# Optimization experiments

Hardware: AMD Instinct MI355X
Metric: run time of the kernel (lower is better)

The kernel has to match this reference:

```python
import jax, jax.numpy as jnp
import numpy as np

# Synthetic base image encoder: patchify(16) -> Linear(768,768)+ReLU -> Linear(768,3072)+ReLU -> mean-pool -> Linear(3072,512)
B, T = 32, 8          # batch, num task vectors
D, DH, F, MH = 768, 3072, 512, 128  # patch dim, hidden, feat_dim, meta-net hidden


def _patchify(x):
    # x: [B,3,224,224] -> [B,196,768] (14x14 patches of 16x16x3)
    Bn = x.shape[0]
    p = x.reshape(Bn, 3, 14, 16, 14, 16).transpose(0, 2, 4, 1, 3, 5)
    return p.reshape(Bn, 196, 768)


def _encode_shared(p, W1, b1, W2, b2, W3, b3):
    h = jax.nn.relu(p @ W1 + b1)          # [B,196,768]
    h2 = jax.nn.relu(h @ W2 + b2)         # [B,196,3072]
    return h2.mean(axis=1) @ W3 + b3      # [B,512]


def setup_inputs() -> dict:
    key = jax.random.key(0)
    ks = jax.random.split(key, 18)
    inp = {"x": jax.random.normal(ks[0], (B, 3, 224, 224), jnp.float32)}
    shapes = {
        "W1": (D, D), "b1": (D,), "W2": (D, DH), "b2": (DH,), "W3": (DH, F), "b3": (F,),
        "dW1": (T, D, D), "db1": (T, D), "dW2": (T, D, DH), "db2": (T, DH),
        "dW3": (T, DH, F), "db3": (T, F),
        "mW1": (F, MH), "mb1": (MH,), "mW2": (MH, T), "mb2": (T,),
    }
    for i, (n, sh) in enumerate(shapes.items()):
        inp[n] = jax.random.normal(ks[i + 1], sh, jnp.float32) * 0.02
    return inp


def reference(x, W1, b1, W2, b2, W3, b3, dW1, db1, dW2, db2, dW3, db3, mW1, mb1, mW2, mb2):
    p = _patchify(x)
    # base features computed with frozen params (torch.no_grad -> stop_gradient)
    base = jax.lax.stop_gradient(_encode_shared(p, W1, b1, W2, b2, W3, b3))
    # MetaNet: Linear-ReLU-Linear -> per-sample task-vector coefficients [B,T]
    coefs = jax.nn.relu(base @ mW1 + mb1) @ mW2 + mb2
    # per-sample composed parameters: theta_b = theta + sum_t coef[b,t] * dtheta_t
    W1b = W1 + jnp.einsum('bt,tde->bde', coefs, dW1)   # [B,768,768]
    b1b = b1 + coefs @ db1
    W2b = W2 + jnp.einsum('bt,tde->bde', coefs, dW2)   # [B,768,3072]
    b2b = b2 + coefs @ db2
    W3b = W3 + jnp.einsum('bt,tdf->bdf', coefs, dW3)   # [B,3072,512]
    b3b = b3 + coefs @ db3
    # batched per-sample forward (replaces the python loop over the batch)
    h = jax.nn.relu(jnp.einsum('bpd,bde->bpe', p, W1b) + b1b[:, None, :])
    h2 = jax.nn.relu(jnp.einsum('bpe,bef->bpf', h, W2b) + b2b[:, None, :])
    return jnp.einsum('be,bef->bf', h2.mean(axis=1), W3b) + b3b  # [B,512]
```

## Files before the change

kernel.cpp:

```cpp
#include <hip/hip_runtime.h>
#include <hip/hip_bf16.h>

#define BATCH 32
#define NPATCH 196
#define PD 768
#define DH 3072
#define FD 512
#define MH 128
#define NT 8

typedef unsigned short u16;
typedef u16   u16x8  __attribute__((ext_vector_type(8)));
typedef short bf16x8 __attribute__((ext_vector_type(8)));
typedef float f32x4  __attribute__((ext_vector_type(4)));

__device__ __forceinline__ void async16(const void* g, void* l)
{
    __builtin_amdgcn_global_load_lds(
        (const __attribute__((address_space(1))) void*)g,
        (__attribute__((address_space(3))) void*)l, 16, 0, 0);
}

#define BARRIER() do { asm volatile("" ::: "memory"); __builtin_amdgcn_s_barrier(); asm volatile("" ::: "memory"); } while (0)
#define VMWAIT(n) asm volatile("s_waitcnt vmcnt(" #n ")" ::: "memory")

#define GK  768
#define NK  24
#define GBM 256
#define GBN 128
#define GBK 32
#define ASZ (GBM*GBK)
#define BSZ (GBN*GBK)

__global__ __launch_bounds__(512, 4)
void gemm_bf16(const u16* __restrict__ A, const u16* __restrict__ BT,
               const float* __restrict__ bias, u16* __restrict__ C,
               float* __restrict__ pooled,
               int M, int N, long sA, long sB, long sC, long sBias,
               int relu, int pool)
{
    const int z = blockIdx.z;
    A  += (long)z * sA;
    BT += (long)z * sB;
    C  += (long)z * sC;
    const float* bz = bias ? bias + (long)z * sBias : nullptr;

    __shared__ __align__(16) u16 As[3 * ASZ];
    __shared__ __align__(16) u16 Bs[3 * BSZ];

    const int tid  = threadIdx.x;
    const int lane = tid & 63;
    const int wave = tid >> 6;
    const int wr = (wave >> 1) * 64;
    const int wc = (wave & 1) * 64;
    const int m0 = blockIdx.y * GBM;
    const int n0 = blockIdx.x * GBN;
    const int lrow = lane & 15;
    const int koff = (lane >> 4) * 8;

    f32x4 acc[4][4] = {};

    auto issue = [&](int kt, int bi) {
        u16* asb = As + bi * ASZ;
        u16* bsb = Bs + bi * BSZ;
        const int k0 = kt * GBK;
#pragma unroll
        for (int r = 0; r < 2; ++r) {
            int chunk = r * 512 + tid;
            int row = chunk >> 2;
            int k8  = chunk & 3;
            int gm  = m0 + row; if (gm >= M) gm = M - 1;
            async16(A + (long)gm * GK + k0 + k8 * 8,
                    asb + (size_t)(r * 512 + wave * 64) * 8);
        }
        int rowb = tid >> 2;
        int k8b  = tid & 3;
        async16(BT + (long)(n0 + rowb) * GK + k0 + k8b * 8,
                bsb + (size_t)(wave * 64) * 8);
    };

    auto compute = [&](int bi) {
        const u16* asb = As + bi * ASZ;
        const u16* bsb = Bs + bi * BSZ;
        bf16x8 af[4], bfr[4];
#pragma unroll
        for (int i = 0; i < 4; ++i)
            af[i] = *(const bf16x8*)(asb + (wr + i * 16 + lrow) * GBK + koff);
#pragma unroll
        for (int j = 0; j < 4; ++j)
            bfr[j] = *(const bf16x8*)(bsb + (wc + j * 16 + lrow) * GBK + koff);
#pragma unroll
        for (int i = 0; i < 4; ++i)
#pragma unroll
            for (int j = 0; j < 4; ++j)
                acc[i][j] = __builtin_amdgcn_mfma_f32_16x16x32_bf16(af[i], bfr[j], acc[i][j], 0, 0, 0);
    };

    issue(0, 0); issue(1, 1); issue(2, 2);

    for (int ii = 0; ii < 7; ++ii) {
        int i0 = ii * 3;
        VMWAIT(6); BARRIER(); compute(0); BARRIER(); issue(i0 + 3, 0);
        VMWAIT(6); BARRIER(); compute(1); BARRIER(); issue(i0 + 4, 1);
        VMWAIT(6); BARRIER(); compute(2); BARRIER(); issue(i0 + 5, 2);
    }
    VMWAIT(6); BARRIER(); compute(0); BARRIER();
    VMWAIT(3); BARRIER(); compute(1); BARRIER();
    VMWAIT(0); BARRIER(); compute(2);

    const int crow = (lane >> 4) * 4;
    const int ccol = lane & 15;

    if (!pool) {
#pragma unroll
        for (int j = 0; j < 4; ++j) {
            int gn = n0 + wc + j * 16 + ccol;
            float bv = bz ? bz[gn] : 0.f;
#pragma unroll
            for (int i = 0; i < 4; ++i) {
#pragma unroll
                for (int rg = 0; rg < 4; ++rg) {
                    int gm = m0 + wr + i * 16 + crow + rg;
                    if (gm < M) {
                        float v = acc[i][j][rg] + bv;
                        if (relu) v = fmaxf(v, 0.f);
                        __hip_bfloat16 hv = __float2bfloat16(v);
                        C[(long)gm * N + gn] = *(u16*)&hv;
                    }
                }
            }
        }
    } else {
        float* poolbuf = (float*)As;
        __syncthreads();
        const int slot = (wave >> 1) * 4 + (lane >> 4);
#pragma unroll
        for (int j = 0; j < 4; ++j) {
            int gn = n0 + wc + j * 16 + ccol;
            float bv = bz ? bz[gn] : 0.f;
            float s = 0.f;
#pragma unroll
            for (int i = 0; i < 4; ++i) {
#pragma unroll
                for (int rg = 0; rg < 4; ++rg) {
                    int gm = wr + i * 16 + crow + rg;
                    if (gm < NPATCH) s += fmaxf(acc[i][j][rg] + bv, 0.f);
                }
            }
            poolbuf[slot * 128 + wc + j * 16 + ccol] = s;
        }
        __syncthreads();
        if (tid < 128) {
            float s = 0.f;
#pragma unroll
            for (int q = 0; q < 16; ++q) s += poolbuf[q * 128 + tid];
            pooled[(long)z * N + n0 + tid] = s * (1.0f / NPATCH);
        }
    }
}

#define L3CHUNK 128

__global__ __launch_bounds__(256)
void skinny3(const float* __restrict__ A, const float* __restrict__ B0,
             const float* __restrict__ dB, const float* __restrict__ cf,
             float* __restrict__ outp, int kchunk)
{
    const int z  = blockIdx.y;
    const int k0 = blockIdx.z * kchunk;
    const float* B = (z == 0) ? B0 : dB + (long)(z - 1) * DH * FD;

    __shared__ float Asl[BATCH][L3CHUNK];

    const int tid = threadIdx.x;
    const int n   = blockIdx.x * 64 + (tid & 63);
    const int bg  = tid >> 6;

    float acc[8] = {};

    for (int kc = 0; kc < kchunk; kc += L3CHUNK) {
#pragma unroll
        for (int r = 0; r < 16; ++r) {
            int idx = tid + r * 256;
            int b = idx >> 7;
            int k = idx & 127;
            float s = (z == 0) ? 1.f : cf[b * NT + z - 1];
            Asl[b][k] = s * A[(long)b * DH + k0 + kc + k];
        }
        __syncthreads();
#pragma unroll 4
        for (int k = 0; k < L3CHUNK; ++k) {
            float w = B[(long)(k0 + kc + k) * FD + n];
#pragma unroll
            for (int bb = 0; bb < 8; ++bb)
                acc[bb] = fmaf(Asl[bg * 8 + bb][k], w, acc[bb]);
        }
        __syncthreads();
    }
#pragma unroll
    for (int bb = 0; bb < 8; ++bb)
        atomicAdd(&outp[(long)(bg * 8 + bb) * FD + n], acc[bb]);
}

__global__ void patchify_bf(const float* __restrict__ x, u16* __restrict__ p, int total)
{
    int i = blockIdx.x * blockDim.x + threadIdx.x;
    if (i >= total) return;
    int d = i % PD;
    int rest = i / PD;
    int patch = rest % NPATCH;
    int b = rest / NPATCH;
    int c = d >> 8;
    int r = (d >> 4) & 15;
    int s = d & 15;
    int pr = patch / 14;
    int pc = patch % 14;
    float v = x[((long)(b * 3 + c) * 224 + (pr * 16 + r)) * 224 + (pc * 16 + s)];
    __hip_bfloat16 hv = __float2bfloat16(v);
    p[i] = *(u16*)&hv;
}

__global__ __launch_bounds__(256)
void wtrans2(const float* __restrict__ W1, u16* __restrict__ o1,
             const float* __restrict__ W2, u16* __restrict__ o2)
{
    const float* W; u16* outp; int K, N, t;
    if (blockIdx.x < 576) { W = W1; outp = o1; K = PD; N = PD;  t = blockIdx.x; }
    else                  { W = W2; outp = o2; K = PD; N = DH;  t = blockIdx.x - 576; }
    int nt = N / 32;
    int k0 = (t / nt) * 32;
    int n0 = (t % nt) * 32;

    __shared__ float Ws[32][33];
    const int tid = threadIdx.x;
#pragma unroll
    for (int r = 0; r < 4; ++r) {
        int idx = tid + r * 256;
        int kk = idx >> 5, nn = idx & 31;
        Ws[kk][nn] = W[(long)(k0 + kk) * N + n0 + nn];
    }
    __syncthreads();
#pragma unroll
    for (int r = 0; r < 4; ++r) {
        int idx = tid + r * 256;
        int kk = idx & 31, nn = idx >> 5;
        __hip_bfloat16 hv = __float2bfloat16(Ws[kk][nn]);
        outp[(long)(n0 + nn) * K + k0 + kk] = *(u16*)&hv;
    }
}

__global__ __launch_bounds__(128)
void compose_w(const float* __restrict__ W, const float* __restrict__ dW,
               const float* __restrict__ cf, u16* __restrict__ out,
               int K, int N)
{
    __shared__ float Ws[9][32][32];
    const int tid = threadIdx.x;
    const int k0 = blockIdx.x * 32;
    const int n0 = blockIdx.y * 32;
    const long tKN = (long)K * N;

#pragma unroll
    for (int a = 0; a < 9; ++a) {
        const float* src = (a == 0) ? W : dW + (long)(a - 1) * tKN;
#pragma unroll
        for (int r = 0; r < 8; ++r) {
            int idx = tid + r * 128;
            int kk = idx >> 5, nn = idx & 31;
            Ws[a][kk][nn] = src[(long)(k0 + kk) * N + n0 + nn];
        }
    }
    __syncthreads();

    const int nn = tid >> 2;
    const int k8 = (tid & 3) * 8;
    float w0[8], d[NT][8];
#pragma unroll
    for (int q = 0; q < 8; ++q) w0[q] = Ws[0][k8 + q][nn];
#pragma unroll
    for (int t = 0; t < NT; ++t)
#pragma unroll
        for (int q = 0; q < 8; ++q) d[t][q] = Ws[t + 1][k8 + q][nn];

    for (int b = 0; b < BATCH; ++b) {
        float c8[NT];
#pragma unroll
        for (int t = 0; t < NT; ++t) c8[t] = cf[b * NT + t];
        u16x8 o;
#pragma unroll
        for (int q = 0; q < 8; ++q) {
            float v = w0[q];
#pragma unroll
            for (int t = 0; t < NT; ++t) v = fmaf(c8[t], d[t][q], v);
            __hip_bfloat16 hv = __float2bfloat16(v);
            o[q] = *(u16*)&hv;
        }
        *(u16x8*)(out + ((long)b * N + (n0 + nn)) * K + k0 + k8) = o;
    }
}

__global__ void compose_bias3(const float* __restrict__ b1, const float* __restrict__ db1,
                              const float* __restrict__ b2, const float* __restrict__ db2,
                              const float* __restrict__ b3, const float* __restrict__ db3,
                              const float* __restrict__ cf,
                              float* __restrict__ o1, float* __restrict__ o2,
                              float* __restrict__ o3)
{
    int i = blockIdx.x * blockDim.x + threadIdx.x;
    const int t1 = BATCH * PD, t2 = BATCH * (PD + DH);
    const float* bs; const float* db; float* o; int N, j;
    if (i < t1)      { bs = b1; db = db1; o = o1; N = PD; j = i; }
    else if (i < t2) { bs = b2; db = db2; o = o2; N = DH; j = i - t1; }
    else {
        j = i - t2;
        if (j >= BATCH * FD) return;
        bs = b3; db = db3; o = o3; N = FD;
    }
    int n = j % N, b = j / N;
    float v = bs[n];
#pragma unroll
    for (int t = 0; t < NT; ++t) v = fmaf(cf[b * NT + t], db[(long)t * N + n], v);
    o[j] = v;
}

__global__ void bias_init(const float* __restrict__ bsrc, float* __restrict__ out, int N)
{
    int i = blockIdx.x * blockDim.x + threadIdx.x;
    if (i >= BATCH * N) return;
    out[i] = bsrc[i % N];
}

__global__ __launch_bounds__(256)
void hid_kernel(const float* __restrict__ base, const float* __restrict__ mW1,
                const float* __restrict__ mb1, float* __restrict__ hid)
{
    int gw   = blockIdx.x * 4 + (threadIdx.x >> 6);
    int lane = threadIdx.x & 63;
    int b = gw >> 7;
    int n = gw & 127;
    float s = 0.f;
#pragma unroll
    for (int i = 0; i < FD / 64; ++i) {
        int k = i * 64 + lane;
        s = fmaf(base[b * FD + k], mW1[k * MH + n], s);
    }
#pragma unroll
    for (int off = 32; off; off >>= 1) s += __shfl_down(s, off, 64);
    if (lane == 0) hid[gw] = fmaxf(s + mb1[n], 0.f);
}

__global__ void coef_kernel(const float* __restrict__ hidden, const float* __restrict__ mW2,
                            const float* __restrict__ mb2, float* __restrict__ coefs)
{
    int i = threadIdx.x;
    int t = i & 7;
    int b = i >> 3;
    float s = mb2[t];
    for (int k = 0; k < MH; ++k)
        s = fmaf(hidden[b * MH + k], mW2[k * NT + t], s);
    coefs[i] = s;
}

extern "C" void kernel_launch(void* const* d_in, const int* in_sizes, int n_in,
                              void* d_out, int out_size, void* d_ws, size_t ws_size,
                              hipStream_t stream)
{
    const float* x   = (const float*)d_in[0];
    const float* W1  = (const float*)d_in[1];
    const float* b1  = (const float*)d_in[2];
    const float* W2  = (const float*)d_in[3];
    const float* b2  = (const float*)d_in[4];
    const float* W3  = (const float*)d_in[5];
    const float* b3  = (const float*)d_in[6];
    const float* dW1 = (const float*)d_in[7];
    const float* db1 = (const float*)d_in[8];
    const float* dW2 = (const float*)d_in[9];
    const float* db2 = (const float*)d_in[10];
    const float* dW3 = (const float*)d_in[11];
    const float* db3 = (const float*)d_in[12];
    const float* mW1 = (const float*)d_in[13];
    const float* mb1 = (const float*)d_in[14];
    const float* mW2 = (const float*)d_in[15];
    const float* mb2 = (const float*)d_in[16];
    float* out = (float*)d_out;
    (void)n_in; (void)in_sizes; (void)out_size; (void)ws_size;

    char* w = (char*)d_ws;
    auto carve = [&](size_t bytes) { void* q = (void*)w; w += (bytes + 255) & ~(size_t)255; return q; };
    const int M1 = BATCH * NPATCH;

    u16*  p_bf  = (u16*)carve((size_t)M1 * PD * 2);
    u16*  h_bf  = (u16*)carve((size_t)M1 * PD * 2);
    u16*  W1T   = (u16*)carve((size_t)PD * PD * 2);
    u16*  W2T   = (u16*)carve((size_t)PD * DH * 2);
    u16*  W1bT  = (u16*)carve((size_t)BATCH * PD * PD * 2);
    u16*  W2bT  = (u16*)carve((size_t)BATCH * DH * PD * 2);
    float* b1b  = (float*)carve((size_t)BATCH * PD * 4);
    float* b2b  = (float*)carve((size_t)BATCH * DH * 4);
    float* h2m  = (float*)carve((size_t)BATCH * DH * 4);
    float* h2m2 = (float*)carve((size_t)BATCH * DH * 4);
    float* base = (float*)carve((size_t)BATCH * FD * 4);
    float* hid  = (float*)carve((size_t)BATCH * MH * 4);
    float* cf   = (float*)carve((size_t)BATCH * NT * 4);

    {
        int total = M1 * PD;
        patchify_bf<<<(total + 255) / 256, 256, 0, stream>>>(x, p_bf, total);
    }
    wtrans2<<<2880, 256, 0, stream>>>(W1, W1T, W2, W2T);
    gemm_bf16<<<dim3(PD / GBN, 25, 1), 512, 0, stream>>>(
        p_bf, W1T, b1, h_bf, nullptr, M1, PD, 0, 0, 0, 0, 1, 0);
    gemm_bf16<<<dim3(DH / GBN, 1, BATCH), 512, 0, stream>>>(
        h_bf, W2T, b2, nullptr, h2m, NPATCH, DH,
        (long)NPATCH * PD, 0, 0, 0, 1, 1);
    bias_init<<<(BATCH * FD + 255) / 256, 256, 0, stream>>>(b3, base, FD);
    skinny3<<<dim3(FD / 64, 1, 24), 256, 0, stream>>>(h2m, W3, nullptr, nullptr, base, DH / 24);
    hid_kernel<<<BATCH * MH / 4, 256, 0, stream>>>(base, mW1, mb1, hid);
    coef_kernel<<<1, 256, 0, stream>>>(hid, mW2, mb2, cf);
    compose_w<<<dim3(PD / 32, PD / 32), 128, 0, stream>>>(W1, dW1, cf, W1bT, PD, PD);
    compose_w<<<dim3(PD / 32, DH / 32), 128, 0, stream>>>(W2, dW2, cf, W2bT, PD, DH);
    compose_bias3<<<(BATCH * (PD + DH + FD) + 255) / 256, 256, 0, stream>>>(
        b1, db1, b2, db2, b3, db3, cf, b1b, b2b, out);
    gemm_bf16<<<dim3(PD / GBN, 1, BATCH), 512, 0, stream>>>(
        p_bf, W1bT, b1b, h_bf, nullptr, NPATCH, PD,
        (long)NPATCH * PD, (long)PD * PD, (long)NPATCH * PD, PD, 1, 0);
    gemm_bf16<<<dim3(DH / GBN, 1, BATCH), 512, 0, stream>>>(
        h_bf, W2bT, b2b, nullptr, h2m2, NPATCH, DH,
        (long)NPATCH * PD, (long)DH * PD, 0, DH, 1, 1);
    skinny3<<<dim3(FD / 64, 9, 6), 256, 0, stream>>>(h2m2, W3, dW3, cf, out, DH / 6);
}
```

Before: 546.0 us.

## Restructure skinny W3 GEMM into register-tiled split-K with partial-sum reduction

The skinny final-layer GEMM kernel now has each thread compute an 8x8 output tile with vectorized float4 weight loads over a 64-wide K slice. The A operand sits transposed in padded shared memory. Per-split partial sums go to a workspace, and a separate reduce kernel adds them and issues one atomic per element instead of many scattered atomics. This is meant to improve weight-load bandwidth, FMA density and parallelism. In exchange it adds an extra kernel launch and a large partial buffer that must be written and read back.

```diff
diff --git a/kernel.cpp b/kernel.cpp
--- a/kernel.cpp
+++ b/kernel.cpp
@@ -159,47 +159,70 @@
     }
 }
 
-#define L3CHUNK 128
+#define SK_KC  64
+#define SK_PAD 36
 
 __global__ __launch_bounds__(256)
 void skinny3(const float* __restrict__ A, const float* __restrict__ B0,
              const float* __restrict__ dB, const float* __restrict__ cf,
-             float* __restrict__ outp, int kchunk)
-{
+             float* __restrict__ partial)
+{
+    const int ks = blockIdx.x;
     const int z  = blockIdx.y;
-    const int k0 = blockIdx.z * kchunk;
+    const int KS = gridDim.x;
+    const int k0 = ks * SK_KC;
     const float* B = (z == 0) ? B0 : dB + (long)(z - 1) * DH * FD;
 
-    __shared__ float Asl[BATCH][L3CHUNK];
-
-    const int tid = threadIdx.x;
-    const int n   = blockIdx.x * 64 + (tid & 63);
-    const int bg  = tid >> 6;
-
-    float acc[8] = {};
-
-    for (int kc = 0; kc < kchunk; kc += L3CHUNK) {
-#pragma unroll
-        for (int r = 0; r < 16; ++r) {
-            int idx = tid + r * 256;
-            int b = idx >> 7;
-            int k = idx & 127;
-            float s = (z == 0) ? 1.f : cf[b * NT + z - 1];
-            Asl[b][k] = s * A[(long)b * DH + k0 + kc + k];
-        }
-        __syncthreads();
-#pragma unroll 4
-        for (int k = 0; k < L3CHUNK; ++k) {
-            float w = B[(long)(k0 + kc + k) * FD + n];
-#pragma unroll
-            for (int bb = 0; bb < 8; ++bb)
-                acc[bb] = fmaf(Asl[bg * 8 + bb][k], w, acc[bb]);
-        }
-        __syncthreads();
-    }
-#pragma unroll
-    for (int bb = 0; bb < 8; ++bb)
-        atomicAdd(&outp[(long)(bg * 8 + bb) * FD + n], acc[bb]);
+    __shared__ __align__(16) float Asl[SK_KC][SK_PAD];
+
+    const int tid  = threadIdx.x;
+    const int nthr = tid & 63;
+    const int bg   = tid >> 6;
+    const int n    = nthr * 8;
+
+    for (int idx = tid; idx < 32 * SK_KC; idx += 256) {
+        int b = idx >> 6;
+        int k = idx & (SK_KC - 1);
+        float sc = (z == 0) ? 1.f : cf[b * NT + (z - 1)];
+        Asl[k][b] = sc * A[(long)b * DH + k0 + k];
+    }
+    __syncthreads();
+
+    f32x4 acc[8][2] = {};
+    for (int k = 0; k < SK_KC; ++k) {
+        const float* bp = B + (long)(k0 + k) * FD + n;
+        f32x4 w0 = *(const f32x4*)bp;
+        f32x4 w1 = *(const f32x4*)(bp + 4);
+        f32x4 a0 = *(const f32x4*)&Asl[k][bg * 8];
+        f32x4 a1 = *(const f32x4*)&Asl[k][bg * 8 + 4];
+#pragma unroll
+        for (int q = 0; q < 4; ++q) {
+#pragma unroll
+            for (int c = 0; c < 4; ++c) {
+                acc[q][0][c]     = fmaf(a0[q], w0[c], acc[q][0][c]);
+                acc[q][1][c]     = fmaf(a0[q], w1[c], acc[q][1][c]);
+                acc[4 + q][0][c] = fmaf(a1[q], w0[c], acc[4 + q][0][c]);
+                acc[4 + q][1][c] = fmaf(a1[q], w1[c], acc[4 + q][1][c]);
+            }
+        }
+    }
+    float* P = partial + ((long)(z * KS + ks) * BATCH + bg * 8) * FD + n;
+#pragma unroll
+    for (int bb = 0; bb < 8; ++bb) {
+        *(f32x4*)(P + (long)bb * FD)     = acc[bb][0];
+        *(f32x4*)(P + (long)bb * FD + 4) = acc[bb][1];
+    }
+}
+
+__global__ __launch_bounds__(256)
+void reduce_partials(const float* __restrict__ partial, float* __restrict__ dst, int per)
+{
+    int i  = blockIdx.x * 256 + threadIdx.x;
+    int p0 = blockIdx.y * per;
+    float s = 0.f;
+    for (int p = 0; p < per; ++p)
+        s += partial[(long)(p0 + p) * (BATCH * FD) + i];
+    atomicAdd(&dst[i], s);
 }
 
 __global__ void patchify_bf(const float* __restrict__ x, u16* __restrict__ p, int total)
@@ -388,6 +411,7 @@
     char* w = (char*)d_ws;
     auto carve = [&](size_t bytes) { void* q = (void*)w; w += (bytes + 255) & ~(size_t)255; return q; };
     const int M1 = BATCH * NPATCH;
+    const int KSPLITS = DH / SK_KC;
 
     u16*  p_bf  = (u16*)carve((size_t)M1 * PD * 2);
     u16*  h_bf  = (u16*)carve((size_t)M1 * PD * 2);
@@ -402,6 +426,7 @@
     float* base = (float*)carve((size_t)BATCH * FD * 4);
     float* hid  = (float*)carve((size_t)BATCH * MH * 4);
     float* cf   = (float*)carve((size_t)BATCH * NT * 4);
+    float* part = (float*)carve((size_t)9 * KSPLITS * BATCH * FD * 4);
 
     {
         int total = M1 * PD;
@@ -414,7 +439,8 @@
         h_bf, W2T, b2, nullptr, h2m, NPATCH, DH,
         (long)NPATCH * PD, 0, 0, 0, 1, 1);
     bias_init<<<(BATCH * FD + 255) / 256, 256, 0, stream>>>(b3, base, FD);
-    skinny3<<<dim3(FD / 64, 1, 24), 256, 0, stream>>>(h2m, W3, nullptr, nullptr, base, DH / 24);
+    skinny3<<<dim3(KSPLITS, 1), 256, 0, stream>>>(h2m, W3, nullptr, nullptr, part);
+    reduce_partials<<<dim3(BATCH * FD / 256, 8), 256, 0, stream>>>(part, base, KSPLITS / 8);
     hid_kernel<<<BATCH * MH / 4, 256, 0, stream>>>(base, mW1, mb1, hid);
     coef_kernel<<<1, 256, 0, stream>>>(hid, mW2, mb2, cf);
     compose_w<<<dim3(PD / 32, PD / 32), 128, 0, stream>>>(W1, dW1, cf, W1bT, PD, PD);
@@ -427,5 +453,6 @@
     gemm_bf16<<<dim3(DH / GBN, 1, BATCH), 512, 0, stream>>>(
         h_bf, W2bT, b2b, nullptr, h2m2, NPATCH, DH,
         (long)NPATCH * PD, (long)DH * PD, 0, DH, 1, 1);
-    skinny3<<<dim3(FD / 64, 9, 6), 256, 0, stream>>>(h2m2, W3, dW3, cf, out, DH / 6);
-}
+    skinny3<<<dim3(KSPLITS, 9), 256, 0, stream>>>(h2m2, W3, dW3, cf, part);
+    reduce_partials<<<dim3(BATCH * FD / 256, 8), 256, 0, stream>>>(part, out, 9 * KSPLITS / 8);
+}
```

After: 521.6 us. 1.05x faster.
